# Optimization experiments

Measured on AMD Instinct MI355X. Metric: run time of the kernel, lower is better.

## Reference

```python
import jax, jax.numpy as jnp
import numpy as np

B, N_N, N_E, C, H = 1, 50000, 250000, 128, 128
NNZ = 2 * N_E


def _layernorm(x, g, b, eps=1e-5):
    mu = jnp.mean(x, axis=-1, keepdims=True)
    var = jnp.mean((x - mu) ** 2, axis=-1, keepdims=True)
    return (x - mu) * jax.lax.rsqrt(var + eps) * g + b


def setup_inputs() -> dict:
    key = jax.random.key(0)
    ks = jax.random.split(key, 12)
    f32 = jnp.float32
    inp = {
        "node": jax.random.normal(ks[0], (B, N_N, C), f32),
        "edge": jax.random.normal(ks[1], (B, N_E, C), f32),
        "edgeIdx": jax.random.randint(ks[2], (N_E, 2), 0, N_N),
        "e2n_rows": jax.random.randint(ks[3], (NNZ,), 0, N_N),
        "e2n_cols": jax.random.randint(ks[4], (NNZ,), 0, N_E),
        "e2n_vals": jnp.ones((NNZ,), f32),
        # norm1 over 3C, norm2 over 2C
        "norm1_g": jnp.ones((3 * C,), f32),
        "norm1_b": jnp.zeros((3 * C,), f32),
        "norm2_g": jnp.ones((2 * C,), f32),
        "norm2_b": jnp.zeros((2 * C,), f32),
        # mlpEdge: 3C -> 3H -> C ; mlpNode: 2C -> 2H -> C (weights stored [in,out])
        "e_w1": jax.random.normal(ks[5], (3 * C, 3 * H), f32) / np.sqrt(3 * C).astype(np.float32),
        "e_b1": jnp.zeros((3 * H,), f32),
        "e_w2": jax.random.normal(ks[6], (3 * H, C), f32) / np.sqrt(3 * H).astype(np.float32),
        "e_b2": jnp.zeros((C,), f32),
        "n_w1": jax.random.normal(ks[7], (2 * C, 2 * H), f32) / np.sqrt(2 * C).astype(np.float32),
        "n_b1": jnp.zeros((2 * H,), f32),
        "n_w2": jax.random.normal(ks[8], (2 * H, C), f32) / np.sqrt(2 * H).astype(np.float32),
        "n_b2": jnp.zeros((C,), f32),
    }
    return inp


def reference(node, edge, edgeIdx, e2n_rows, e2n_cols, e2n_vals,
              norm1_g, norm1_b, norm2_g, norm2_b,
              e_w1, e_b1, e_w2, e_b2, n_w1, n_b1, n_w2, n_b2):
    Bv, Nn, Cc = node.shape
    Ne = edge.shape[1]
    # gather both endpoints of each edge: [B, N_e, 2, C] -> [B, N_e, 2C]
    gathered = node[:, edgeIdx].reshape(Bv, Ne, 2 * Cc)
    e = jnp.concatenate([edge, gathered], axis=-1)           # [B, N_e, 3C]
    e = _layernorm(e, norm1_g, norm1_b)
    e = jax.nn.gelu(e @ e_w1 + e_b1, approximate=False) @ e_w2 + e_b2  # [B, N_e, C]
    e_h = e.astype(jnp.float16)                              # matches .half() in torch
    # sparse matmul edge2node @ edge  == scatter-add over COO nnz
    msg = e_h.transpose(1, 0, 2)[e2n_cols] * e2n_vals.astype(jnp.float16)[:, None, None]  # [nnz, B, C]
    agg = jax.ops.segment_sum(msg, e2n_rows, num_segments=Nn)  # [N_n, B, C]
    node_agg = agg.transpose(1, 0, 2).astype(node.dtype)       # [B, N_n, C]
    n = jnp.concatenate([node, node_agg], axis=-1)             # [B, N_n, 2C]
    n = _layernorm(n, norm2_g, norm2_b)
    n = jax.nn.gelu(n @ n_w1 + n_b1, approximate=False) @ n_w2 + n_b2
    node_out = node + n
    edge_out = edge + e_h.astype(edge.dtype)
    return node_out, edge_out
```

## Files before the change

### kernel.cpp

```cpp
#include <hip/hip_runtime.h>
#include <hip/hip_fp16.h>

typedef unsigned short u16;
typedef unsigned int u32;

#define N_NODE 50000
#define N_EDGE 250000
#define NNZV   500000

typedef __attribute__((ext_vector_type(8))) __bf16 bf16x8;
typedef __attribute__((ext_vector_type(4))) float f32x4;

#define WAITLGKM0() asm volatile("s_waitcnt lgkmcnt(0)" ::: "memory")
#define SBAR() __builtin_amdgcn_s_barrier()
#define SCHEDB() __builtin_amdgcn_sched_barrier(0)

static __device__ __forceinline__ u16 f2bf(float f) {
  union { float f; u32 u; } cv; cv.f = f;
  u32 u = cv.u;
  return (u16)((u + 0x7FFFu + ((u >> 16) & 1u)) >> 16);
}

static __device__ __forceinline__ u32 pk_bf16(float lo, float hi) {
  u32 r;
  asm("v_cvt_pk_bf16_f32 %0, %1, %2" : "=v"(r) : "v"(lo), "v"(hi));
  return r;
}

static __device__ __forceinline__ u16 f2bf_fast(float x) {
  return (u16)pk_bf16(x, x);
}

template<typename T>
static __device__ __forceinline__ T ldo(const void* base, u32 off) {
  return *(const T*)((const char*)base + off);
}
template<typename T>
static __device__ __forceinline__ void sto(void* base, u32 off, T v) {
  *(T*)((char*)base + off) = v;
}

static __device__ __forceinline__ float gelu_f(float x) {
  float z = fabsf(x) * 0.70710678118654752f;
  float t = __builtin_amdgcn_rcpf(1.0f + 0.3275911f * z);
  float p = t * (0.254829592f + t * (-0.284496736f + t * (1.421413741f +
            t * (-1.453152027f + t * 1.061405429f))));
  float er = 1.0f - p * __expf(-z * z);
  er = copysignf(er, x);
  return 0.5f * x * (1.0f + er);
}

static __device__ __forceinline__ void wconv(const float* __restrict__ in,
                                             u16* __restrict__ out,
                                             int K, int N, int cpw, int idx) {
  int k = idx / N, n = idx % N;
  int w = n / cpw, rem = n % cpw;
  int t = rem >> 4, l15 = rem & 15;
  int ks = k >> 5, gq = (k >> 3) & 3, e = k & 7;
  int steps = K >> 5, tiles = cpw >> 4;
  size_t o = ((((size_t)(w * steps + ks) * tiles + t) * 64) + gq * 16 + l15) * 8 + e;
  out[o] = f2bf(in[(size_t)k * N + n]);
}

__global__ __launch_bounds__(256) void prep_kernel(
    const float* __restrict__ ew1, const float* __restrict__ ew2,
    const float* __restrict__ nw1, const float* __restrict__ nw2,
    u16* __restrict__ ew1r, u16* __restrict__ ew2r,
    u16* __restrict__ nw1r, u16* __restrict__ nw2r,
    u32* __restrict__ agg0) {
  const int S1 = 384 * 384, S2 = 384 * 128, S3 = 256 * 256, S4 = 256 * 128;
  const int SA = N_NODE * 128 / 2;
  const long total = (long)S1 + S2 + S3 + S4 + SA;
  for (long i = (long)blockIdx.x * 256 + threadIdx.x; i < total;
       i += (long)gridDim.x * 256) {
    long idx = i;
    if (idx < S1) { wconv(ew1, ew1r, 384, 384, 48, (int)idx); continue; }
    idx -= S1;
    if (idx < S2) { wconv(ew2, ew2r, 384, 128, 16, (int)idx); continue; }
    idx -= S2;
    if (idx < S3) { wconv(nw1, nw1r, 256, 256, 32, (int)idx); continue; }
    idx -= S3;
    if (idx < S4) { wconv(nw2, nw2r, 256, 128, 16, (int)idx); continue; }
    idx -= S4;
    agg0[idx] = 0;
  }
}

__global__ __launch_bounds__(512, 4) void edge_fused_kernel(
    const float* __restrict__ node, const float* __restrict__ edge,
    const int* __restrict__ edgeIdx,
    const float* __restrict__ lng, const float* __restrict__ lnb,
    const u16* __restrict__ w1r, const float* __restrict__ b1,
    const u16* __restrict__ w2r, const float* __restrict__ b2,
    __half* __restrict__ e_h, float* __restrict__ out_edge, int store_eh) {
  const int lane = threadIdx.x & 63, wid = threadIdx.x >> 6;
  const int l15 = lane & 15, gq = lane >> 4;
  const int row0 = blockIdx.x * 64;

  __shared__ __align__(16) u16 xp[64 * 384];
  __shared__ __align__(16) float er[64 * 128];

  const bf16x8* w1v = (const bf16x8*)w1r + (size_t)wid * (12 * 192) + lane;
  bf16x8 br[3][3];
#define LDB1(s, b) { br[b][0] = w1v[(s) * 192]; br[b][1] = w1v[(s) * 192 + 64]; \
                     br[b][2] = w1v[(s) * 192 + 128]; }
  LDB1(0, 0); LDB1(1, 1); LDB1(2, 2);

  float ga[6], be[6];
#pragma unroll
  for (int s = 0; s < 3; ++s) {
    float2 g2 = *(const float2*)&lng[s * 128 + 2 * lane];
    float2 b2v = *(const float2*)&lnb[s * 128 + 2 * lane];
    ga[2 * s] = g2.x; ga[2 * s + 1] = g2.y;
    be[2 * s] = b2v.x; be[2 * s + 1] = b2v.y;
  }
  {
    u32 oe[8], oa[8], ob[8];
#pragma unroll
    for (int t = 0; t < 8; ++t) {
      int g = row0 + wid * 8 + t; if (g > N_EDGE - 1) g = N_EDGE - 1;
      int2 ab = ldo<int2>(edgeIdx, (u32)g * 8);
      oe[t] = (u32)g * 512 + lane * 8;
      oa[t] = (u32)ab.x * 512 + lane * 8;
      ob[t] = (u32)ab.y * 512 + lane * 8;
    }
    float2 v0[8], v1[8], v2[8];
#pragma unroll
    for (int t = 0; t < 8; ++t) {
      v0[t] = ldo<float2>(edge, oe[t]);
      v1[t] = ldo<float2>(node, oa[t]);
      v2[t] = ldo<float2>(node, ob[t]);
    }
#pragma unroll
    for (int t = 0; t < 8; ++t) {
      int lr = wid * 8 + t;
      *(float2*)&er[lr * 128 + 2 * lane] = v0[t];
      float s  = v0[t].x + v0[t].y + v1[t].x + v1[t].y + v2[t].x + v2[t].y;
      float ss = v0[t].x*v0[t].x + v0[t].y*v0[t].y + v1[t].x*v1[t].x +
                 v1[t].y*v1[t].y + v2[t].x*v2[t].x + v2[t].y*v2[t].y;
#pragma unroll
      for (int m = 1; m < 64; m <<= 1) { s += __shfl_xor(s, m); ss += __shfl_xor(ss, m); }
      float mean = s * (1.0f / 384.0f);
      float var  = ss * (1.0f / 384.0f) - mean * mean;
      float rstd = rsqrtf(var + 1e-5f);
      float2 vv[3] = {v0[t], v1[t], v2[t]};
#pragma unroll
      for (int sg = 0; sg < 3; ++sg) {
        float y0 = (vv[sg].x - mean) * rstd * ga[2 * sg]     + be[2 * sg];
        float y1 = (vv[sg].y - mean) * rstd * ga[2 * sg + 1] + be[2 * sg + 1];
        int sl = (sg * 16 + (lane >> 2)) ^ (lr & 15);
        *(u32*)&xp[lr * 384 + sl * 8 + (lane & 3) * 2] = pk_bf16(y0, y1);
      }
    }
  }
  WAITLGKM0(); SCHEDB(); SBAR(); SCHEDB();

  f32x4 acc1[4][3];
#pragma unroll
  for (int nt = 0; nt < 3; ++nt) {
    float bv = b1[wid * 48 + nt * 16 + l15];
#pragma unroll
    for (int m = 0; m < 4; ++m) acc1[m][nt] = (f32x4){bv, bv, bv, bv};
  }
  int aoff[4];
#pragma unroll
  for (int m = 0; m < 4; ++m) aoff[m] = (m * 16 + l15) * 384;

#pragma unroll
  for (int s = 0; s < 12; ++s) {
    const int axi = ((s * 4 + gq) ^ l15) * 8;
    bf16x8 a[4];
#pragma unroll
    for (int m = 0; m < 4; ++m) a[m] = *(const bf16x8*)&xp[aoff[m] + axi];
    __builtin_amdgcn_s_setprio(1);
#pragma unroll
    for (int m = 0; m < 4; ++m)
#pragma unroll
      for (int nt = 0; nt < 3; ++nt)
        acc1[m][nt] = __builtin_amdgcn_mfma_f32_16x16x32_bf16(a[m], br[s % 3][nt], acc1[m][nt], 0, 0, 0);
    __builtin_amdgcn_s_setprio(0);
    if (s + 3 < 12) { LDB1(s + 3, s % 3); }
  }
  SCHEDB(); SBAR(); SCHEDB();

  const bf16x8* w2v = (const bf16x8*)w2r + (size_t)wid * (12 * 64) + lane;
  bf16x8 br2[3];
#define LDB2(s, b) { br2[b] = w2v[(s) * 64]; }
  LDB2(0, 0); LDB2(1, 1); LDB2(2, 2);
#pragma unroll
  for (int m = 0; m < 4; ++m)
#pragma unroll
    for (int nt = 0; nt < 3; ++nt) {
      const int c = wid * 48 + nt * 16 + l15;
#pragma unroll
      for (int j = 0; j < 4; ++j) {
        int r = m * 16 + gq * 4 + j;
        xp[r * 384 + (((c >> 3) ^ (r & 15)) * 8) + (c & 7)] = f2bf_fast(gelu_f(acc1[m][nt][j]));
      }
    }
  WAITLGKM0(); SCHEDB(); SBAR(); SCHEDB();

  float b2v = b2[wid * 16 + l15];
  f32x4 acc2[4];
#pragma unroll
  for (int m = 0; m < 4; ++m) acc2[m] = (f32x4){b2v, b2v, b2v, b2v};

#pragma unroll
  for (int g = 0; g < 12; ++g) {
    const int axi = ((g * 4 + gq) ^ l15) * 8;
    bf16x8 a[4];
#pragma unroll
    for (int m = 0; m < 4; ++m) a[m] = *(const bf16x8*)&xp[aoff[m] + axi];
    __builtin_amdgcn_s_setprio(1);
#pragma unroll
    for (int m = 0; m < 4; ++m)
      acc2[m] = __builtin_amdgcn_mfma_f32_16x16x32_bf16(a[m], br2[g % 3], acc2[m], 0, 0, 0);
    __builtin_amdgcn_s_setprio(0);
    if (g + 3 < 12) { LDB2(g + 3, g % 3); }
  }

  const int col = wid * 16 + l15;
#pragma unroll
  for (int m = 0; m < 4; ++m)
#pragma unroll
    for (int j = 0; j < 4; ++j) {
      int lr = m * 16 + gq * 4 + j;
      int r = row0 + lr;
      if (r < N_EDGE) {
        __half hv = __float2half(acc2[m][j]);
        if (store_eh) sto<__half>(e_h, (u32)r * 256 + col * 2, hv);
        sto<float>(out_edge, (u32)r * 512 + col * 4, er[lr * 128 + col] + __half2float(hv));
      }
    }
#undef LDB1
#undef LDB2
}

__global__ __launch_bounds__(512, 4) void node_fused_kernel(
    const float* __restrict__ node, const __half* __restrict__ agg,
    const float* __restrict__ lng, const float* __restrict__ lnb,
    const u16* __restrict__ w1r, const float* __restrict__ b1,
    const u16* __restrict__ w2r, const float* __restrict__ b2,
    float* __restrict__ out_node) {
  const int lane = threadIdx.x & 63, wid = threadIdx.x >> 6;
  const int l15 = lane & 15, gq = lane >> 4;
  const int row0 = blockIdx.x * 64;

  __shared__ __align__(16) u16 xp[64 * 256];
  __shared__ __align__(16) float nr[64 * 128];

  const bf16x8* w1v = (const bf16x8*)w1r + (size_t)wid * (8 * 128) + lane;
  bf16x8 br[3][2];
#define NLDB1(s, b) { br[b][0] = w1v[(s) * 128]; br[b][1] = w1v[(s) * 128 + 64]; }
  NLDB1(0, 0); NLDB1(1, 1); NLDB1(2, 2);

  float ga[4], be[4];
#pragma unroll
  for (int s = 0; s < 2; ++s) {
    float2 g2 = *(const float2*)&lng[s * 128 + 2 * lane];
    float2 b2v = *(const float2*)&lnb[s * 128 + 2 * lane];
    ga[2 * s] = g2.x; ga[2 * s + 1] = g2.y;
    be[2 * s] = b2v.x; be[2 * s + 1] = b2v.y;
  }
  {
    float2 v0[8], v1[8];
#pragma unroll
    for (int t = 0; t < 8; ++t) {
      int g = row0 + wid * 8 + t; if (g > N_NODE - 1) g = N_NODE - 1;
      v0[t] = ldo<float2>(node, (u32)g * 512 + lane * 8);
      v1[t] = __half22float2(ldo<__half2>(agg, (u32)g * 256 + lane * 4));
    }
#pragma unroll
    for (int t = 0; t < 8; ++t) {
      int lr = wid * 8 + t;
      *(float2*)&nr[lr * 128 + 2 * lane] = v0[t];
      float s  = v0[t].x + v0[t].y + v1[t].x + v1[t].y;
      float ss = v0[t].x*v0[t].x + v0[t].y*v0[t].y + v1[t].x*v1[t].x + v1[t].y*v1[t].y;
#pragma unroll
      for (int m = 1; m < 64; m <<= 1) { s += __shfl_xor(s, m); ss += __shfl_xor(ss, m); }
      float mean = s * (1.0f / 256.0f);
      float var  = ss * (1.0f / 256.0f) - mean * mean;
      float rstd = rsqrtf(var + 1e-5f);
      float2 vv[2] = {v0[t], v1[t]};
#pragma unroll
      for (int sg = 0; sg < 2; ++sg) {
        float y0 = (vv[sg].x - mean) * rstd * ga[2 * sg]     + be[2 * sg];
        float y1 = (vv[sg].y - mean) * rstd * ga[2 * sg + 1] + be[2 * sg + 1];
        int sl = (sg * 16 + (lane >> 2)) ^ (lr & 15);
        *(u32*)&xp[lr * 256 + sl * 8 + (lane & 3) * 2] = pk_bf16(y0, y1);
      }
    }
  }
  WAITLGKM0(); SCHEDB(); SBAR(); SCHEDB();

  f32x4 acc1[4][2];
#pragma unroll
  for (int nt = 0; nt < 2; ++nt) {
    float bv = b1[wid * 32 + nt * 16 + l15];
#pragma unroll
    for (int m = 0; m < 4; ++m) acc1[m][nt] = (f32x4){bv, bv, bv, bv};
  }
  int aoff[4];
#pragma unroll
  for (int m = 0; m < 4; ++m) aoff[m] = (m * 16 + l15) * 256;

#pragma unroll
  for (int s = 0; s < 8; ++s) {
    const int axi = ((s * 4 + gq) ^ l15) * 8;
    bf16x8 a[4];
#pragma unroll
    for (int m = 0; m < 4; ++m) a[m] = *(const bf16x8*)&xp[aoff[m] + axi];
    __builtin_amdgcn_s_setprio(1);
#pragma unroll
    for (int m = 0; m < 4; ++m)
#pragma unroll
      for (int nt = 0; nt < 2; ++nt)
        acc1[m][nt] = __builtin_amdgcn_mfma_f32_16x16x32_bf16(a[m], br[s % 3][nt], acc1[m][nt], 0, 0, 0);
    __builtin_amdgcn_s_setprio(0);
    if (s + 3 < 8) { NLDB1(s + 3, s % 3); }
  }
  SCHEDB(); SBAR(); SCHEDB();

  const bf16x8* w2v = (const bf16x8*)w2r + (size_t)wid * (8 * 64) + lane;
  bf16x8 br2[3];
#define NLDB2(s, b) { br2[b] = w2v[(s) * 64]; }
  NLDB2(0, 0); NLDB2(1, 1); NLDB2(2, 2);
#pragma unroll
  for (int m = 0; m < 4; ++m)
#pragma unroll
    for (int nt = 0; nt < 2; ++nt) {
      const int c = wid * 32 + nt * 16 + l15;
#pragma unroll
      for (int j = 0; j < 4; ++j) {
        int r = m * 16 + gq * 4 + j;
        xp[r * 256 + (((c >> 3) ^ (r & 15)) * 8) + (c & 7)] = f2bf_fast(gelu_f(acc1[m][nt][j]));
      }
    }
  WAITLGKM0(); SCHEDB(); SBAR(); SCHEDB();

  float b2v = b2[wid * 16 + l15];
  f32x4 acc2[4];
#pragma unroll
  for (int m = 0; m < 4; ++m) acc2[m] = (f32x4){b2v, b2v, b2v, b2v};

#pragma unroll
  for (int g = 0; g < 8; ++g) {
    const int axi = ((g * 4 + gq) ^ l15) * 8;
    bf16x8 a[4];
#pragma unroll
    for (int m = 0; m < 4; ++m) a[m] = *(const bf16x8*)&xp[aoff[m] + axi];
    __builtin_amdgcn_s_setprio(1);
#pragma unroll
    for (int m = 0; m < 4; ++m)
      acc2[m] = __builtin_amdgcn_mfma_f32_16x16x32_bf16(a[m], br2[g % 3], acc2[m], 0, 0, 0);
    __builtin_amdgcn_s_setprio(0);
    if (g + 3 < 8) { NLDB2(g + 3, g % 3); }
  }

  const int col = wid * 16 + l15;
#pragma unroll
  for (int m = 0; m < 4; ++m)
#pragma unroll
    for (int j = 0; j < 4; ++j) {
      int lr = m * 16 + gq * 4 + j;
      int r = row0 + lr;
      if (r < N_NODE) {
        sto<float>(out_node, (u32)r * 512 + col * 4, nr[lr * 128 + col] + acc2[m][j]);
      }
    }
#undef NLDB1
#undef NLDB2
}

__global__ __launch_bounds__(256) void scatter_kernel(
    const int* __restrict__ rows, const int* __restrict__ cols,
    const float* __restrict__ vals,
    const __half* __restrict__ e_h,
    const float* __restrict__ out_edge, const float* __restrict__ edge,
    __half* __restrict__ agg, int use_eh) {
  int k = __builtin_amdgcn_readfirstlane(blockIdx.x * 4 + (threadIdx.x >> 6));
  int l = threadIdx.x & 63;
  int r = rows[k], c = cols[k];
  float v = vals[k];
  __half2 h2;
  if (use_eh) {
    h2 = *(const __half2*)&e_h[(size_t)c * 128 + 2 * l];
  } else {
    size_t o = (size_t)c * 128 + 2 * l;
    float2 eo = *(const float2*)&out_edge[o];
    float2 e0 = *(const float2*)&edge[o];
    h2 = __floats2half2_rn(eo.x - e0.x, eo.y - e0.y);
  }
  h2 = __hmul2(h2, __float2half2_rn(v));
  unsafeAtomicAdd((__half2*)&agg[(size_t)r * 128 + 2 * l], h2);
}

extern "C" void kernel_launch(void* const* d_in, const int* in_sizes, int n_in,
                              void* d_out, int out_size, void* d_ws, size_t ws_size,
                              hipStream_t stream) {
  (void)in_sizes; (void)n_in; (void)out_size;
  const float* node    = (const float*)d_in[0];
  const float* edge    = (const float*)d_in[1];
  const int*   edgeIdx = (const int*)d_in[2];
  const int*   e2n_r   = (const int*)d_in[3];
  const int*   e2n_c   = (const int*)d_in[4];
  const float* e2n_v   = (const float*)d_in[5];
  const float* n1g     = (const float*)d_in[6];
  const float* n1b     = (const float*)d_in[7];
  const float* n2g     = (const float*)d_in[8];
  const float* n2b     = (const float*)d_in[9];
  const float* ew1     = (const float*)d_in[10];
  const float* eb1     = (const float*)d_in[11];
  const float* ew2     = (const float*)d_in[12];
  const float* eb2     = (const float*)d_in[13];
  const float* nw1     = (const float*)d_in[14];
  const float* nb1     = (const float*)d_in[15];
  const float* nw2     = (const float*)d_in[16];
  const float* nb2     = (const float*)d_in[17];

  float* out_node = (float*)d_out;
  float* out_edge = out_node + (size_t)N_NODE * 128;

  char* w = (char*)d_ws;
  auto alloc = [&](size_t bytes) { char* p = w; w += (bytes + 255) & ~(size_t)255; return p; };
  u16* ew1r = (u16*)alloc((size_t)384 * 384 * 2);
  u16* ew2r = (u16*)alloc((size_t)384 * 128 * 2);
  u16* nw1r = (u16*)alloc((size_t)256 * 256 * 2);
  u16* nw2r = (u16*)alloc((size_t)256 * 128 * 2);
  __half* agg = (__half*)alloc((size_t)N_NODE * 128 * 2);

  size_t used = (size_t)(w - (char*)d_ws);
  const size_t EH_BYTES = (size_t)N_EDGE * 128 * 2;
  int use_eh = (ws_size >= used + EH_BYTES) ? 1 : 0;
  __half* e_h = nullptr;
  if (use_eh) e_h = (__half*)alloc(EH_BYTES);

  prep_kernel<<<1024, 256, 0, stream>>>(ew1, ew2, nw1, nw2,
                                        ew1r, ew2r, nw1r, nw2r, (u32*)agg);

  edge_fused_kernel<<<(N_EDGE + 63) / 64, 512, 0, stream>>>(
      node, edge, edgeIdx, n1g, n1b, ew1r, eb1, ew2r, eb2, e_h, out_edge, use_eh);

  scatter_kernel<<<(NNZV + 3) / 4, 256, 0, stream>>>(
      e2n_r, e2n_c, e2n_v, e_h, out_edge, edge, agg, use_eh);

  node_fused_kernel<<<(N_NODE + 63) / 64, 512, 0, stream>>>(
      node, agg, n2g, n2b, nw1r, nb1, nw2r, nb2, out_node);
}
```

Before: 345.2 us.

## Fuse scatter-add into edge kernel via per-edge bucketed COO index

Adds a fill pass that buckets COO entries by edge column (fixed capacity per edge, with an overflow list), then has the edge kernel stage its fp16 output in shared memory and scatter-add it directly into the node aggregate. The standalone scatter kernel and the global fp16 edge buffer round-trip are removed. Entries beyond bucket capacity go to a small overflow kernel. Costs are an extra atomic fill pass, a large bucket buffer, scatter work serialised per wave inside the edge kernel, and silent drops if overflow exceeds its cap.

```diff
diff --git a/kernel.cpp b/kernel.cpp
--- a/kernel.cpp
+++ b/kernel.cpp
@@ -7,6 +7,8 @@
 #define N_NODE 50000
 #define N_EDGE 250000
 #define NNZV   500000
+#define BCAP   24
+#define OVFCAP 4096
 
 typedef __attribute__((ext_vector_type(8))) __bf16 bf16x8;
 typedef __attribute__((ext_vector_type(4))) float f32x4;
@@ -67,10 +69,11 @@
     const float* __restrict__ nw1, const float* __restrict__ nw2,
     u16* __restrict__ ew1r, u16* __restrict__ ew2r,
     u16* __restrict__ nw1r, u16* __restrict__ nw2r,
-    u32* __restrict__ agg0) {
+    u32* __restrict__ agg0, u32* __restrict__ cnt0) {
   const int S1 = 384 * 384, S2 = 384 * 128, S3 = 256 * 256, S4 = 256 * 128;
   const int SA = N_NODE * 128 / 2;
-  const long total = (long)S1 + S2 + S3 + S4 + SA;
+  const int SC = N_EDGE + 1;
+  const long total = (long)S1 + S2 + S3 + S4 + SA + SC;
   for (long i = (long)blockIdx.x * 256 + threadIdx.x; i < total;
        i += (long)gridDim.x * 256) {
     long idx = i;
@@ -82,7 +85,43 @@
     idx -= S3;
     if (idx < S4) { wconv(nw2, nw2r, 256, 128, 16, (int)idx); continue; }
     idx -= S4;
-    agg0[idx] = 0;
+    if (idx < SA) { agg0[idx] = 0; continue; }
+    idx -= SA;
+    cnt0[idx] = 0;
+  }
+}
+
+__global__ __launch_bounds__(256) void fill_kernel(
+    const int* __restrict__ rows, const int* __restrict__ cols,
+    const float* __restrict__ vals,
+    u32* __restrict__ cnt, int2* __restrict__ buck, int4* __restrict__ ovf) {
+  int k = blockIdx.x * 256 + threadIdx.x;
+  if (k >= NNZV) return;
+  int c = cols[k];
+  u32 p = atomicAdd(&cnt[c], 1u);
+  if (p < BCAP) {
+    buck[(size_t)c * BCAP + p] = make_int2(rows[k], __float_as_int(vals[k]));
+  } else {
+    u32 q = atomicAdd(&cnt[N_EDGE], 1u);
+    if (q < OVFCAP) ovf[q] = make_int4(rows[k], c, __float_as_int(vals[k]), 0);
+  }
+}
+
+__global__ __launch_bounds__(256) void ovf_scatter_kernel(
+    const int4* __restrict__ ovf, const u32* __restrict__ cnt,
+    const float* __restrict__ out_edge, const float* __restrict__ edge,
+    __half* __restrict__ agg) {
+  int n = (int)cnt[N_EDGE]; if (n > OVFCAP) n = OVFCAP;
+  int wv = blockIdx.x * 4 + (threadIdx.x >> 6);
+  int l = threadIdx.x & 63;
+  for (int q = wv; q < n; q += gridDim.x * 4) {
+    int4 e = ovf[q];
+    size_t o = (size_t)e.y * 128 + 2 * l;
+    float2 eo = *(const float2*)&out_edge[o];
+    float2 e0 = *(const float2*)&edge[o];
+    __half2 h2 = __floats2half2_rn(eo.x - e0.x, eo.y - e0.y);
+    h2 = __hmul2(h2, __float2half2_rn(__int_as_float(e.z)));
+    unsafeAtomicAdd((__half2*)&agg[(size_t)e.x * 128 + 2 * l], h2);
   }
 }
 
@@ -92,7 +131,8 @@
     const float* __restrict__ lng, const float* __restrict__ lnb,
     const u16* __restrict__ w1r, const float* __restrict__ b1,
     const u16* __restrict__ w2r, const float* __restrict__ b2,
-    __half* __restrict__ e_h, float* __restrict__ out_edge, int store_eh) {
+    const u32* __restrict__ cnt, const int2* __restrict__ buck,
+    __half* __restrict__ agg, float* __restrict__ out_edge) {
   const int lane = threadIdx.x & 63, wid = threadIdx.x >> 6;
   const int l15 = lane & 15, gq = lane >> 4;
   const int row0 = blockIdx.x * 64;
@@ -228,10 +268,34 @@
       int r = row0 + lr;
       if (r < N_EDGE) {
         __half hv = __float2half(acc2[m][j]);
-        if (store_eh) sto<__half>(e_h, (u32)r * 256 + col * 2, hv);
         sto<float>(out_edge, (u32)r * 512 + col * 4, er[lr * 128 + col] + __half2float(hv));
       }
     }
+
+  __half* ehl = (__half*)er;
+  WAITLGKM0(); SCHEDB(); SBAR(); SCHEDB();
+#pragma unroll
+  for (int m = 0; m < 4; ++m)
+#pragma unroll
+    for (int j = 0; j < 4; ++j) {
+      int lr = m * 16 + gq * 4 + j;
+      ehl[lr * 128 + col] = __float2half(acc2[m][j]);
+    }
+  WAITLGKM0(); SCHEDB(); SBAR(); SCHEDB();
+
+  for (int t = 0; t < 8; ++t) {
+    int lrow = wid * 8 + t;
+    int r = row0 + lrow;
+    if (r >= N_EDGE) break;
+    u32 rf = __builtin_amdgcn_readfirstlane((u32)r);
+    u32 n = cnt[rf]; if (n > BCAP) n = BCAP;
+    __half2 hh = *(__half2*)&ehl[lrow * 128 + 2 * lane];
+    for (u32 p = 0; p < n; ++p) {
+      int2 e = buck[(size_t)rf * BCAP + p];
+      __half2 h2 = __hmul2(hh, __float2half2_rn(__int_as_float(e.y)));
+      unsafeAtomicAdd((__half2*)&agg[(size_t)e.x * 128 + 2 * lane], h2);
+    }
+  }
 #undef LDB1
 #undef LDB2
 }
@@ -372,33 +436,10 @@
 #undef NLDB2
 }
 
-__global__ __launch_bounds__(256) void scatter_kernel(
-    const int* __restrict__ rows, const int* __restrict__ cols,
-    const float* __restrict__ vals,
-    const __half* __restrict__ e_h,
-    const float* __restrict__ out_edge, const float* __restrict__ edge,
-    __half* __restrict__ agg, int use_eh) {
-  int k = __builtin_amdgcn_readfirstlane(blockIdx.x * 4 + (threadIdx.x >> 6));
-  int l = threadIdx.x & 63;
-  int r = rows[k], c = cols[k];
-  float v = vals[k];
-  __half2 h2;
-  if (use_eh) {
-    h2 = *(const __half2*)&e_h[(size_t)c * 128 + 2 * l];
-  } else {
-    size_t o = (size_t)c * 128 + 2 * l;
-    float2 eo = *(const float2*)&out_edge[o];
-    float2 e0 = *(const float2*)&edge[o];
-    h2 = __floats2half2_rn(eo.x - e0.x, eo.y - e0.y);
-  }
-  h2 = __hmul2(h2, __float2half2_rn(v));
-  unsafeAtomicAdd((__half2*)&agg[(size_t)r * 128 + 2 * l], h2);
-}
-
 extern "C" void kernel_launch(void* const* d_in, const int* in_sizes, int n_in,
                               void* d_out, int out_size, void* d_ws, size_t ws_size,
                               hipStream_t stream) {
-  (void)in_sizes; (void)n_in; (void)out_size;
+  (void)in_sizes; (void)n_in; (void)out_size; (void)ws_size;
   const float* node    = (const float*)d_in[0];
   const float* edge    = (const float*)d_in[1];
   const int*   edgeIdx = (const int*)d_in[2];
@@ -428,21 +469,21 @@
   u16* nw1r = (u16*)alloc((size_t)256 * 256 * 2);
   u16* nw2r = (u16*)alloc((size_t)256 * 128 * 2);
   __half* agg = (__half*)alloc((size_t)N_NODE * 128 * 2);
-
-  size_t used = (size_t)(w - (char*)d_ws);
-  const size_t EH_BYTES = (size_t)N_EDGE * 128 * 2;
-  int use_eh = (ws_size >= used + EH_BYTES) ? 1 : 0;
-  __half* e_h = nullptr;
-  if (use_eh) e_h = (__half*)alloc(EH_BYTES);
+  u32* cnt  = (u32*)alloc((size_t)(N_EDGE + 1) * 4);
+  int4* ovf = (int4*)alloc((size_t)OVFCAP * 16);
+  int2* buck = (int2*)alloc((size_t)N_EDGE * BCAP * 8);
 
   prep_kernel<<<1024, 256, 0, stream>>>(ew1, ew2, nw1, nw2,
-                                        ew1r, ew2r, nw1r, nw2r, (u32*)agg);
+                                        ew1r, ew2r, nw1r, nw2r, (u32*)agg, cnt);
+
+  fill_kernel<<<(NNZV + 255) / 256, 256, 0, stream>>>(
+      e2n_r, e2n_c, e2n_v, cnt, buck, ovf);
 
   edge_fused_kernel<<<(N_EDGE + 63) / 64, 512, 0, stream>>>(
-      node, edge, edgeIdx, n1g, n1b, ew1r, eb1, ew2r, eb2, e_h, out_edge, use_eh);
-
-  scatter_kernel<<<(NNZV + 3) / 4, 256, 0, stream>>>(
-      e2n_r, e2n_c, e2n_v, e_h, out_edge, edge, agg, use_eh);
+      node, edge, edgeIdx, n1g, n1b, ew1r, eb1, ew2r, eb2,
+      cnt, buck, agg, out_edge);
+
+  ovf_scatter_kernel<<<16, 256, 0, stream>>>(ovf, cnt, out_edge, edge, agg);
 
   node_fused_kernel<<<(N_NODE + 63) / 64, 512, 0, stream>>>(
       node, agg, n2g, n2b, nw1r, nb1, nw2r, nb2, out_node);
```

Measured after the change: 345.4 us. About the same (+0.1%).

## Replace atomic scatter with row-bucketed gather aggregation for edge-to-node sum

Applied to the files above, without the earlier changes.

Builds per-node buckets of (col,val) pairs with an atomic counter pass, then aggregates each node's messages in registers with fp32 accumulation and a single fp16 store, instead of 500k wavefront-level half2 atomics into agg. Rows with more than 48 entries go to a small overflow list handled by an atomic scatter kernel. It also drops the fallback path that recomputed e_h from out_edge, assuming the workspace is large enough. Accumulating in fp32 changes rounding relative to the fp16 atomics, and entries beyond the overflow capacity would be silently dropped.

```diff
diff --git a/kernel.cpp b/kernel.cpp
--- a/kernel.cpp
+++ b/kernel.cpp
@@ -7,6 +7,8 @@
 #define N_NODE 50000
 #define N_EDGE 250000
 #define NNZV   500000
+#define RCAP   48
+#define OVFCAP 4096
 
 typedef __attribute__((ext_vector_type(8))) __bf16 bf16x8;
 typedef __attribute__((ext_vector_type(4))) float f32x4;
@@ -67,10 +69,10 @@
     const float* __restrict__ nw1, const float* __restrict__ nw2,
     u16* __restrict__ ew1r, u16* __restrict__ ew2r,
     u16* __restrict__ nw1r, u16* __restrict__ nw2r,
-    u32* __restrict__ agg0) {
+    u32* __restrict__ rcnt0) {
   const int S1 = 384 * 384, S2 = 384 * 128, S3 = 256 * 256, S4 = 256 * 128;
-  const int SA = N_NODE * 128 / 2;
-  const long total = (long)S1 + S2 + S3 + S4 + SA;
+  const int SC = N_NODE + 1;
+  const long total = (long)S1 + S2 + S3 + S4 + SC;
   for (long i = (long)blockIdx.x * 256 + threadIdx.x; i < total;
        i += (long)gridDim.x * 256) {
     long idx = i;
@@ -82,7 +84,56 @@
     idx -= S3;
     if (idx < S4) { wconv(nw2, nw2r, 256, 128, 16, (int)idx); continue; }
     idx -= S4;
-    agg0[idx] = 0;
+    rcnt0[idx] = 0;
+  }
+}
+
+__global__ __launch_bounds__(256) void fill_row_kernel(
+    const int* __restrict__ rows, const int* __restrict__ cols,
+    const float* __restrict__ vals,
+    u32* __restrict__ rcnt, int2* __restrict__ buck, int4* __restrict__ ovf) {
+  int k = blockIdx.x * 256 + threadIdx.x;
+  if (k >= NNZV) return;
+  int r = rows[k];
+  u32 p = atomicAdd(&rcnt[r], 1u);
+  if (p < RCAP) {
+    buck[(size_t)r * RCAP + p] = make_int2(cols[k], __float_as_int(vals[k]));
+  } else {
+    u32 q = atomicAdd(&rcnt[N_NODE], 1u);
+    if (q < OVFCAP) ovf[q] = make_int4(r, cols[k], __float_as_int(vals[k]), 0);
+  }
+}
+
+__global__ __launch_bounds__(256) void agg_gather_kernel(
+    const u32* __restrict__ rcnt, const int2* __restrict__ buck,
+    const __half* __restrict__ e_h, __half* __restrict__ agg) {
+  int r = __builtin_amdgcn_readfirstlane(blockIdx.x * 4 + (threadIdx.x >> 6));
+  if (r >= N_NODE) return;
+  int l = threadIdx.x & 63;
+  u32 n = rcnt[r]; if (n > RCAP) n = RCAP;
+  float a0 = 0.0f, a1 = 0.0f;
+  for (u32 p = 0; p < n; ++p) {
+    int2 e = buck[(size_t)r * RCAP + p];
+    __half2 hv = *(const __half2*)&e_h[(size_t)e.x * 128 + 2 * l];
+    float v = __int_as_float(e.y);
+    float2 f = __half22float2(hv);
+    a0 = fmaf(f.x, v, a0);
+    a1 = fmaf(f.y, v, a1);
+  }
+  *(__half2*)&agg[(size_t)r * 128 + 2 * l] = __floats2half2_rn(a0, a1);
+}
+
+__global__ __launch_bounds__(256) void ovf_scatter_kernel(
+    const int4* __restrict__ ovf, const u32* __restrict__ rcnt,
+    const __half* __restrict__ e_h, __half* __restrict__ agg) {
+  int n = (int)rcnt[N_NODE]; if (n > OVFCAP) n = OVFCAP;
+  int wv = blockIdx.x * 4 + (threadIdx.x >> 6);
+  int l = threadIdx.x & 63;
+  for (int q = wv; q < n; q += gridDim.x * 4) {
+    int4 e = ovf[q];
+    __half2 hv = *(const __half2*)&e_h[(size_t)e.y * 128 + 2 * l];
+    __half2 h2 = __hmul2(hv, __float2half2_rn(__int_as_float(e.z)));
+    unsafeAtomicAdd((__half2*)&agg[(size_t)e.x * 128 + 2 * l], h2);
   }
 }
 
@@ -92,7 +143,7 @@
     const float* __restrict__ lng, const float* __restrict__ lnb,
     const u16* __restrict__ w1r, const float* __restrict__ b1,
     const u16* __restrict__ w2r, const float* __restrict__ b2,
-    __half* __restrict__ e_h, float* __restrict__ out_edge, int store_eh) {
+    __half* __restrict__ e_h, float* __restrict__ out_edge) {
   const int lane = threadIdx.x & 63, wid = threadIdx.x >> 6;
   const int l15 = lane & 15, gq = lane >> 4;
   const int row0 = blockIdx.x * 64;
@@ -228,7 +279,7 @@
       int r = row0 + lr;
       if (r < N_EDGE) {
         __half hv = __float2half(acc2[m][j]);
-        if (store_eh) sto<__half>(e_h, (u32)r * 256 + col * 2, hv);
+        sto<__half>(e_h, (u32)r * 256 + col * 2, hv);
         sto<float>(out_edge, (u32)r * 512 + col * 4, er[lr * 128 + col] + __half2float(hv));
       }
     }
@@ -372,33 +423,10 @@
 #undef NLDB2
 }
 
-__global__ __launch_bounds__(256) void scatter_kernel(
-    const int* __restrict__ rows, const int* __restrict__ cols,
-    const float* __restrict__ vals,
-    const __half* __restrict__ e_h,
-    const float* __restrict__ out_edge, const float* __restrict__ edge,
-    __half* __restrict__ agg, int use_eh) {
-  int k = __builtin_amdgcn_readfirstlane(blockIdx.x * 4 + (threadIdx.x >> 6));
-  int l = threadIdx.x & 63;
-  int r = rows[k], c = cols[k];
-  float v = vals[k];
-  __half2 h2;
-  if (use_eh) {
-    h2 = *(const __half2*)&e_h[(size_t)c * 128 + 2 * l];
-  } else {
-    size_t o = (size_t)c * 128 + 2 * l;
-    float2 eo = *(const float2*)&out_edge[o];
-    float2 e0 = *(const float2*)&edge[o];
-    h2 = __floats2half2_rn(eo.x - e0.x, eo.y - e0.y);
-  }
-  h2 = __hmul2(h2, __float2half2_rn(v));
-  unsafeAtomicAdd((__half2*)&agg[(size_t)r * 128 + 2 * l], h2);
-}
-
 extern "C" void kernel_launch(void* const* d_in, const int* in_sizes, int n_in,
                               void* d_out, int out_size, void* d_ws, size_t ws_size,
                               hipStream_t stream) {
-  (void)in_sizes; (void)n_in; (void)out_size;
+  (void)in_sizes; (void)n_in; (void)out_size; (void)ws_size;
   const float* node    = (const float*)d_in[0];
   const float* edge    = (const float*)d_in[1];
   const int*   edgeIdx = (const int*)d_in[2];
@@ -428,21 +456,23 @@
   u16* nw1r = (u16*)alloc((size_t)256 * 256 * 2);
   u16* nw2r = (u16*)alloc((size_t)256 * 128 * 2);
   __half* agg = (__half*)alloc((size_t)N_NODE * 128 * 2);
-
-  size_t used = (size_t)(w - (char*)d_ws);
-  const size_t EH_BYTES = (size_t)N_EDGE * 128 * 2;
-  int use_eh = (ws_size >= used + EH_BYTES) ? 1 : 0;
-  __half* e_h = nullptr;
-  if (use_eh) e_h = (__half*)alloc(EH_BYTES);
+  __half* e_h = (__half*)alloc((size_t)N_EDGE * 128 * 2);
+  u32* rcnt = (u32*)alloc((size_t)(N_NODE + 1) * 4);
+  int4* ovf = (int4*)alloc((size_t)OVFCAP * 16);
+  int2* buck = (int2*)alloc((size_t)N_NODE * RCAP * 8);
 
   prep_kernel<<<1024, 256, 0, stream>>>(ew1, ew2, nw1, nw2,
-                                        ew1r, ew2r, nw1r, nw2r, (u32*)agg);
+                                        ew1r, ew2r, nw1r, nw2r, rcnt);
+
+  fill_row_kernel<<<(NNZV + 255) / 256, 256, 0, stream>>>(
+      e2n_r, e2n_c, e2n_v, rcnt, buck, ovf);
 
   edge_fused_kernel<<<(N_EDGE + 63) / 64, 512, 0, stream>>>(
-      node, edge, edgeIdx, n1g, n1b, ew1r, eb1, ew2r, eb2, e_h, out_edge, use_eh);
-
-  scatter_kernel<<<(NNZV + 3) / 4, 256, 0, stream>>>(
-      e2n_r, e2n_c, e2n_v, e_h, out_edge, edge, agg, use_eh);
+      node, edge, edgeIdx, n1g, n1b, ew1r, eb1, ew2r, eb2, e_h, out_edge);
+
+  agg_gather_kernel<<<(N_NODE + 3) / 4, 256, 0, stream>>>(rcnt, buck, e_h, agg);
+
+  ovf_scatter_kernel<<<16, 256, 0, stream>>>(ovf, rcnt, e_h, agg);
 
   node_fused_kernel<<<(N_NODE + 63) / 64, 512, 0, stream>>>(
       node, agg, n2g, n2b, nw1r, nb1, nw2r, nb2, out_node);
```

Result: faster. 306.1 us (-11.3%).
